# Optimization experiments

Measured on AMD Instinct MI355X. Metric: run time of the kernel, lower is better.

Reference implementation:

```python
import jax, jax.numpy as jnp
import numpy as np

RADIUS = 0.25  # module init arg


def _spp(x):
    """Spatial pyramid max pooling over the (K=8, C) plane.
    x: [B, N, 8, C] -> [B, N, 21] (4x4 + 2x2 + 1x1 bins)."""
    B, N, K, C = x.shape
    outs = []
    for h, w in ((4, 4), (2, 2), (1, 1)):
        r = x.reshape(B, N, h, K // h, w, C // w)
        outs.append(r.max(axis=(3, 5)).reshape(B, N, h * w))
    return jnp.concatenate(outs, axis=-1)


def _pointsift_select(xyz, radius):
    """Octant-wise nearest-neighbor selection. xyz: [Bp, N, 3] -> idx [Bp, N, 8]."""
    Bp, N, _ = xyz.shape
    judge = radius * radius
    # diff[b, n, m] = xyz[b, m] - xyz[b, n]  (point m relative to centroid n)
    diff = xyz[:, None, :, :] - xyz[:, :, None, :]          # [Bp, N, N, 3]
    dist = jnp.sum(diff * diff, axis=-1)                     # [Bp, N, N]
    octw = jnp.array([4, 2, 1], dtype=jnp.int32)
    sub = jnp.sum((diff + 1.0).astype(jnp.int32) * octw, -1)  # [Bp, N, N] octant id
    valid = (dist > 1e-10) & (dist < judge)
    eye = jnp.eye(N, dtype=bool)                             # self entry gets judge_dist
    idxs = []
    for i in range(8):
        d_i = jnp.where(valid & (sub == i), dist, 1e10)
        d_i = jnp.where(eye, judge, d_i)
        idxs.append(jnp.argmin(d_i, axis=-1))                # first-min, matches torch
    return jnp.stack(idxs, axis=-1)                          # [Bp, N, 8]


def setup_inputs() -> dict:
    key = jax.random.key(0)
    ks = jax.random.split(key, 7)
    C = 256
    x = jax.random.uniform(ks[0], (2, 2, 2048, 3), dtype=jnp.float32)
    w1 = jax.random.normal(ks[1], (C, 3), dtype=jnp.float32) * 0.05
    b1 = jax.random.normal(ks[2], (C,), dtype=jnp.float32) * 0.05
    w2 = jax.random.normal(ks[3], (C, C), dtype=jnp.float32) * 0.05
    b2 = jax.random.normal(ks[4], (C,), dtype=jnp.float32) * 0.05
    w3 = jax.random.normal(ks[5], (C, C), dtype=jnp.float32) * 0.05
    b3 = jax.random.normal(ks[6], (C,), dtype=jnp.float32) * 0.05
    return {"x": x, "w1": w1, "b1": b1, "w2": w2, "b2": b2, "w3": w3, "b3": b3}


def reference(x, w1, b1, w2, b2, w3, b3):
    B, T, N, _ = x.shape
    xyz = x.reshape(B * T, N, 3)
    idx = _pointsift_select(xyz, RADIUS)                     # [Bp, N, 8]
    b_idx = jnp.arange(B * T)[:, None, None]
    grouped = xyz[b_idx, idx] - xyz[:, :, None, :]           # [Bp, N, 8, 3] relative coords
    # three stacked 1x1 convs (no nonlinearity, per original Sequential)
    h = jnp.einsum('bnkc,oc->bnko', grouped, w1) + b1
    h = jnp.einsum('bnkc,oc->bnko', h, w2) + b2
    h = jnp.einsum('bnkc,oc->bnko', h, w3) + b3              # [Bp, N, 8, C]
    out = _spp(h)                                            # [Bp, N, 21]
    return out.reshape(B, T, N, -1)
```

## Files before the change

### kernel.cpp

```cpp
#include <hip/hip_runtime.h>

#define NPTS 2048
#define CCH  256
#define CAP  320
#define CAPU (CAP - 64)

template <int CTRL>
__device__ __forceinline__ float dppf(float v) {
    return __int_as_float(__builtin_amdgcn_update_dpp(
        0, __float_as_int(v), CTRL, 0xF, 0xF, true));
}
__device__ __forceinline__ float row16_max(float v) {
    v = fmaxf(v, dppf<0xB1>(v));
    v = fmaxf(v, dppf<0x4E>(v));
    v = fmaxf(v, dppf<0x141>(v));
    v = fmaxf(v, dppf<0x140>(v));
    return v;
}
__device__ __forceinline__ float row16_min(float v) {
    v = fminf(v, dppf<0xB1>(v));
    v = fminf(v, dppf<0x4E>(v));
    v = fminf(v, dppf<0x141>(v));
    v = fminf(v, dppf<0x140>(v));
    return v;
}
__device__ __forceinline__ float row16_sum(float v) {
    v += dppf<0xB1>(v);
    v += dppf<0x4E>(v);
    v += dppf<0x141>(v);
    v += dppf<0x140>(v);
    return v;
}
__device__ __forceinline__ float wave_sum(float v) {
    v = row16_sum(v);
    v += __shfl_xor(v, 16, 64);
    v += __shfl_xor(v, 32, 64);
    return v;
}

__device__ __forceinline__ int cell_coord(float v) {
    int c = (int)(v * 4.0f);
    return min(3, max(0, c));
}


__global__ __launch_bounds__(256) void prep_kernel(
    const float* __restrict__ w1, const float* __restrict__ b1,
    const float* __restrict__ w2, const float* __restrict__ b2,
    const float* __restrict__ w3, const float* __restrict__ b3,
    float* __restrict__ ws)
{
    __shared__ float  w3row[2][CCH];
    __shared__ float4 wpart[2][4];
    int o0 = blockIdx.x * 2, c = threadIdx.x;

    float w3c0 = w3[(o0 + 0) * CCH + c];
    float w3c1 = w3[(o0 + 1) * CCH + c];
    w3row[0][c] = w3c0;
    w3row[1][c] = w3c1;
    __syncthreads();

    float a0 = 0.f, a1 = 0.f, a2 = 0.f, a3 = 0.f;
    float b0 = 0.f, b1p = 0.f, b2p = 0.f, b3p = 0.f;
    const float* w2c = w2 + c;
    for (int k = 0; k < CCH; k += 4) {
        float q0 = w2c[(k + 0) * CCH];
        float q1 = w2c[(k + 1) * CCH];
        float q2 = w2c[(k + 2) * CCH];
        float q3 = w2c[(k + 3) * CCH];
        a0 = fmaf(w3row[0][k + 0], q0, a0);
        a1 = fmaf(w3row[0][k + 1], q1, a1);
        a2 = fmaf(w3row[0][k + 2], q2, a2);
        a3 = fmaf(w3row[0][k + 3], q3, a3);
        b0  = fmaf(w3row[1][k + 0], q0, b0);
        b1p = fmaf(w3row[1][k + 1], q1, b1p);
        b2p = fmaf(w3row[1][k + 2], q2, b2p);
        b3p = fmaf(w3row[1][k + 3], q3, b3p);
    }
    float accA = (a0 + a1) + (a2 + a3);
    float accB = (b0 + b1p) + (b2p + b3p);

    float w1x = w1[c * 3 + 0], w1y = w1[c * 3 + 1], w1z = w1[c * 3 + 2];
    float b1c = b1[c], b2c = b2[c];

    float4 vA = make_float4(accA * w1x, accA * w1y, accA * w1z,
                            fmaf(accA, b1c, w3c0 * b2c));
    float4 vB = make_float4(accB * w1x, accB * w1y, accB * w1z,
                            fmaf(accB, b1c, w3c1 * b2c));
    vA.x = wave_sum(vA.x); vA.y = wave_sum(vA.y);
    vA.z = wave_sum(vA.z); vA.w = wave_sum(vA.w);
    vB.x = wave_sum(vB.x); vB.y = wave_sum(vB.y);
    vB.z = wave_sum(vB.z); vB.w = wave_sum(vB.w);
    if ((c & 63) == 0) {
        wpart[0][c >> 6] = vA;
        wpart[1][c >> 6] = vB;
    }
    __syncthreads();
    if (c < 2) {
        int o = o0 + c;
        float4 p0 = wpart[c][0], p1 = wpart[c][1], p2 = wpart[c][2], p3 = wpart[c][3];
        ws[o * 3 + 0] = (p0.x + p1.x) + (p2.x + p3.x);
        ws[o * 3 + 1] = (p0.y + p1.y) + (p2.y + p3.y);
        ws[o * 3 + 2] = (p0.z + p1.z) + (p2.z + p3.z);
        ws[3 * CCH + o] = (p0.w + p1.w) + (p2.w + p3.w) + b3[o];
    }
}

__global__ __launch_bounds__(1024) void pointsift_kernel(
    const float* __restrict__ x,
    const float* __restrict__ ws,
    float* __restrict__ out)
{
    __shared__ float4 scrd[NPTS];
    __shared__ unsigned sstart[66];
    __shared__ unsigned shist[64];
    __shared__ unsigned scur[64];
    __shared__ unsigned short slist[16][CAP];

    int tid = threadIdx.x;
    int batch = blockIdx.x >> 7;
    int n0    = (blockIdx.x & 127) * 16;
    const float* xb = x + (size_t)batch * NPTS * 3;

    if (tid < 64) shist[tid] = 0;
    __syncthreads();

    float2 f0 = *(const float2*)(xb + 6 * tid + 0);
    float2 f1 = *(const float2*)(xb + 6 * tid + 2);
    float2 f2 = *(const float2*)(xb + 6 * tid + 4);
    float3 p0 = make_float3(f0.x, f0.y, f1.x);
    float3 p1 = make_float3(f1.y, f2.x, f2.y);
    int c0 = (cell_coord(p0.x) << 4) | (cell_coord(p0.y) << 2) | cell_coord(p0.z);
    int c1 = (cell_coord(p1.x) << 4) | (cell_coord(p1.y) << 2) | cell_coord(p1.z);
    atomicAdd(&shist[c0], 1u);
    atomicAdd(&shist[c1], 1u);
    __syncthreads();

    if (tid < 64) {
        unsigned v = shist[tid];
        unsigned incl = v;
#pragma unroll
        for (int s = 1; s < 64; s <<= 1) {
            unsigned o = __shfl_up(incl, s, 64);
            if (tid >= s) incl += o;
        }
        unsigned excl = incl - v;
        sstart[tid] = excl;
        scur[tid] = excl;
        if (tid == 63) sstart[64] = NPTS;
    }
    __syncthreads();

    {
        unsigned q0 = atomicAdd(&scur[c0], 1u);
        scrd[q0] = make_float4(p0.x, p0.y, p0.z, __uint_as_float(2u * tid));
        unsigned q1 = atomicAdd(&scur[c1], 1u);
        scrd[q1] = make_float4(p1.x, p1.y, p1.z, __uint_as_float(2u * tid + 1u));
    }

    int wave = tid >> 6;
    int lane = tid & 63;
    int n = n0 + wave;

    float3 cpt = *(const float3*)(xb + 3 * n);
    float cx = cpt.x, cy = cpt.y, cz = cpt.z;

    __syncthreads();

    int ccx = cell_coord(cx), ccy = cell_coord(cy), ccz = cell_coord(cz);
    int zlo = ccz > 0 ? ccz - 1 : 0;
    int zhi = ccz < 3 ? ccz + 1 : 3;

    unsigned short* slw = slist[wave];

    unsigned cnt = 0;
    for (int di = -1; di <= 1; ++di) {
        int a = ccx + di;
        if ((unsigned)a > 3u) continue;
        for (int dj = -1; dj <= 1; ++dj) {
            int bc = ccy + dj;
            if ((unsigned)bc > 3u) continue;
            int base = (a << 4) | (bc << 2);
            unsigned s0 = sstart[base + zlo];
            unsigned e0 = sstart[base + zhi + 1];
            for (unsigned pp = s0; pp < e0; pp += 64) {
                unsigned pos = pp + lane;
                bool inb = pos < e0;
                float4 p = scrd[inb ? pos : 0];
                float dx = p.x - cx, dy = p.y - cy, dz = p.z - cz;
                float d2 = __fadd_rn(__fadd_rn(__fmul_rn(dx, dx), __fmul_rn(dy, dy)),
                                     __fmul_rn(dz, dz));
                bool valid = inb && (d2 > 1e-10f) && (d2 < 0.0625f);
                unsigned long long mask = __ballot(valid);
                if (valid && cnt <= CAPU) {
                    unsigned below = __builtin_amdgcn_mbcnt_hi(
                        (unsigned)(mask >> 32),
                        __builtin_amdgcn_mbcnt_lo((unsigned)mask, 0u));
                    slw[cnt + below] = (unsigned short)pos;
                }
                cnt += (unsigned)__popcll(mask);
            }
        }
    }

    unsigned long long bk[8];
#pragma unroll
    for (int i = 0; i < 8; ++i)
        bk[i] = (0x7f800000ULL << 32) | (unsigned)n;

    if (cnt <= CAPU) {
        int cn = (int)cnt;
        for (int t = lane; t < cn; t += 64) {
            int pos = slw[t];
            float4 p = scrd[pos];
            unsigned m = __float_as_uint(p.w);
            float dx = p.x - cx, dy = p.y - cy, dz = p.z - cz;
            float d2 = __fadd_rn(__fadd_rn(__fmul_rn(dx, dx), __fmul_rn(dy, dy)),
                                 __fmul_rn(dz, dz));
            int oct = 4 * (int)(dx + 1.0f) + 2 * (int)(dy + 1.0f) + (int)(dz + 1.0f);
            unsigned long long key =
                ((unsigned long long)__float_as_uint(d2) << 32) | m;
#pragma unroll
            for (int i = 0; i < 8; ++i) {
                bool upd = (oct == i) && (key < bk[i]);
                bk[i] = upd ? key : bk[i];
            }
        }
    } else {
        for (int pos = lane; pos < NPTS; pos += 64) {
            float4 p = scrd[pos];
            unsigned m = __float_as_uint(p.w);
            float dx = p.x - cx, dy = p.y - cy, dz = p.z - cz;
            float d2 = __fadd_rn(__fadd_rn(__fmul_rn(dx, dx), __fmul_rn(dy, dy)),
                                 __fmul_rn(dz, dz));
            bool valid = (d2 > 1e-10f) && (d2 < 0.0625f);
            int oct = 4 * (int)(dx + 1.0f) + 2 * (int)(dy + 1.0f) + (int)(dz + 1.0f);
            unsigned long long key =
                ((unsigned long long)__float_as_uint(d2) << 32) | m;
#pragma unroll
            for (int i = 0; i < 8; ++i) {
                bool upd = valid && (oct == i) && (key < bk[i]);
                bk[i] = upd ? key : bk[i];
            }
        }
    }

    int nidx[8];
#pragma unroll
    for (int i = 0; i < 8; ++i) {
        float bdf = __uint_as_float((unsigned)(bk[i] >> 32));
        int   bii = (int)(unsigned)bk[i];
        float mv = row16_min(bdf);
        mv = fminf(mv, __shfl_xor(mv, 16, 64));
        mv = fminf(mv, __shfl_xor(mv, 32, 64));
        unsigned long long mk = __ballot(bdf == mv);
        if (__popcll(mk) == 1) {
            nidx[i] = __builtin_amdgcn_readlane(bii, (int)__builtin_ctzll(mk));
        } else {
            int mm = (bdf == mv) ? bii : 0x7FFFFFFF;
#pragma unroll
            for (int s = 32; s > 0; s >>= 1) {
                int o = __shfl_xor(mm, s, 64);
                mm = o < mm ? o : mm;
            }
            nidx[i] = mm;
        }
    }

    const float4* wsv = (const float4*)ws;
    float4 wa = wsv[lane * 3 + 0];
    float4 wb = wsv[lane * 3 + 1];
    float4 wc = wsv[lane * 3 + 2];
    float4 be = ((const float4*)(ws + 3 * CCH))[lane];
    float w[4][3] = {{wa.x, wa.y, wa.z}, {wa.w, wb.x, wb.y},
                     {wb.z, wb.w, wc.x}, {wc.y, wc.z, wc.w}};
    float bev[4] = {be.x, be.y, be.z, be.w};

    float m16[4];
#pragma unroll
    for (int i = 0; i < 4; ++i) m16[i] = -__builtin_inff();
#pragma unroll
    for (int k = 0; k < 8; ++k) {
        float3 p = *(const float3*)(xb + 3 * nidx[k]);
        float gx = p.x - cx, gy = p.y - cy, gz = p.z - cz;
#pragma unroll
        for (int q = 0; q < 4; ++q) {
            float h = fmaf(gx, w[q][0], fmaf(gy, w[q][1], fmaf(gz, w[q][2], bev[q])));
            m16[k >> 1] = fmaxf(m16[k >> 1], h);
        }
    }

    float t[4], u[4];
#pragma unroll
    for (int i = 0; i < 4; ++i) {
        m16[i] = row16_max(m16[i]);
        t[i] = fmaxf(m16[i], __shfl_xor(m16[i], 16, 64));
        u[i] = fmaxf(t[i], __shfl_xor(t[i], 32, 64));
    }

    float* op = out + ((size_t)batch * NPTS + n) * 21;
    if ((lane & 15) == 0) {
        int j = lane >> 4;
#pragma unroll
        for (int i = 0; i < 4; ++i)
            op[i * 4 + j] = m16[i];
    }
    if (lane == 0 || lane == 32) {
        int j2 = lane >> 5;
        op[16 + 0 * 2 + j2] = fmaxf(t[0], t[1]);
        op[16 + 1 * 2 + j2] = fmaxf(t[2], t[3]);
    }
    if (lane == 0) {
        op[20] = fmaxf(fmaxf(u[0], u[1]), fmaxf(u[2], u[3]));
    }
}

extern "C" void kernel_launch(void* const* d_in, const int* in_sizes, int n_in,
                              void* d_out, int out_size, void* d_ws, size_t ws_size,
                              hipStream_t stream) {
    const float* x  = (const float*)d_in[0];
    const float* w1 = (const float*)d_in[1];
    const float* b1 = (const float*)d_in[2];
    const float* w2 = (const float*)d_in[3];
    const float* b2 = (const float*)d_in[4];
    const float* w3 = (const float*)d_in[5];
    const float* b3 = (const float*)d_in[6];
    float* out = (float*)d_out;
    float* ws  = (float*)d_ws;

    prep_kernel<<<CCH / 2, CCH, 0, stream>>>(w1, b1, w2, b2, w3, b3, ws);

    int Bp = in_sizes[0] / (NPTS * 3);
    pointsift_kernel<<<Bp * (NPTS / 16), 1024, 0, stream>>>(x, ws, out);
}
```

Measured before the change: 26.33 us.

## Replace neighbor list compaction and wave reductions with LDS atomic-min per octant

Each wave now keeps eight packed (distance, index) keys in shared memory, one per octant. Candidates in the neighboring grid cells update those keys directly with a 64-bit workgroup-scope atomic min. This removes the ballot-compacted neighbor list, the second candidate pass, the dense fallback scan over all points, and the per-octant cross-lane min reductions. In exchange, lanes that hit the same octant now contend on LDS atomics, and correctness relies on the wave's own LDS atomics being visible to its later reads without an explicit barrier.

New measurement: 22.15 us, median of 2. 1.19x faster.

```diff
diff --git a/kernel.cpp b/kernel.cpp
--- a/kernel.cpp
+++ b/kernel.cpp
@@ -2,8 +2,6 @@
 
 #define NPTS 2048
 #define CCH  256
-#define CAP  320
-#define CAPU (CAP - 64)
 
 template <int CTRL>
 __device__ __forceinline__ float dppf(float v) {
@@ -15,13 +13,6 @@
     v = fmaxf(v, dppf<0x4E>(v));
     v = fmaxf(v, dppf<0x141>(v));
     v = fmaxf(v, dppf<0x140>(v));
-    return v;
-}
-__device__ __forceinline__ float row16_min(float v) {
-    v = fminf(v, dppf<0xB1>(v));
-    v = fminf(v, dppf<0x4E>(v));
-    v = fminf(v, dppf<0x141>(v));
-    v = fminf(v, dppf<0x140>(v));
     return v;
 }
 __device__ __forceinline__ float row16_sum(float v) {
@@ -115,7 +106,7 @@
     __shared__ unsigned sstart[66];
     __shared__ unsigned shist[64];
     __shared__ unsigned scur[64];
-    __shared__ unsigned short slist[16][CAP];
+    __shared__ unsigned long long soct[16][8];
 
     int tid = threadIdx.x;
     int batch = blockIdx.x >> 7;
@@ -165,15 +156,15 @@
     float3 cpt = *(const float3*)(xb + 3 * n);
     float cx = cpt.x, cy = cpt.y, cz = cpt.z;
 
+    if (lane < 8)
+        soct[wave][lane] = (0x7f800000ULL << 32) | (unsigned)n;
+
     __syncthreads();
 
     int ccx = cell_coord(cx), ccy = cell_coord(cy), ccz = cell_coord(cz);
     int zlo = ccz > 0 ? ccz - 1 : 0;
     int zhi = ccz < 3 ? ccz + 1 : 3;
 
-    unsigned short* slw = slist[wave];
-
-    unsigned cnt = 0;
     for (int di = -1; di <= 1; ++di) {
         int a = ccx + di;
         if ((unsigned)a > 3u) continue;
@@ -183,89 +174,28 @@
             int base = (a << 4) | (bc << 2);
             unsigned s0 = sstart[base + zlo];
             unsigned e0 = sstart[base + zhi + 1];
-            for (unsigned pp = s0; pp < e0; pp += 64) {
-                unsigned pos = pp + lane;
-                bool inb = pos < e0;
-                float4 p = scrd[inb ? pos : 0];
+            for (unsigned pp = s0 + lane; pp < e0; pp += 64) {
+                float4 p = scrd[pp];
                 float dx = p.x - cx, dy = p.y - cy, dz = p.z - cz;
                 float d2 = __fadd_rn(__fadd_rn(__fmul_rn(dx, dx), __fmul_rn(dy, dy)),
                                      __fmul_rn(dz, dz));
-                bool valid = inb && (d2 > 1e-10f) && (d2 < 0.0625f);
-                unsigned long long mask = __ballot(valid);
-                if (valid && cnt <= CAPU) {
-                    unsigned below = __builtin_amdgcn_mbcnt_hi(
-                        (unsigned)(mask >> 32),
-                        __builtin_amdgcn_mbcnt_lo((unsigned)mask, 0u));
-                    slw[cnt + below] = (unsigned short)pos;
+                if ((d2 > 1e-10f) && (d2 < 0.0625f)) {
+                    int oct = 4 * (int)(dx + 1.0f) + 2 * (int)(dy + 1.0f) + (int)(dz + 1.0f);
+                    unsigned long long key =
+                        ((unsigned long long)__float_as_uint(d2) << 32) |
+                        __float_as_uint(p.w);
+                    __hip_atomic_fetch_min(&soct[wave][oct], key,
+                                           __ATOMIC_RELAXED,
+                                           __HIP_MEMORY_SCOPE_WORKGROUP);
                 }
-                cnt += (unsigned)__popcll(mask);
             }
         }
     }
 
-    unsigned long long bk[8];
-#pragma unroll
-    for (int i = 0; i < 8; ++i)
-        bk[i] = (0x7f800000ULL << 32) | (unsigned)n;
-
-    if (cnt <= CAPU) {
-        int cn = (int)cnt;
-        for (int t = lane; t < cn; t += 64) {
-            int pos = slw[t];
-            float4 p = scrd[pos];
-            unsigned m = __float_as_uint(p.w);
-            float dx = p.x - cx, dy = p.y - cy, dz = p.z - cz;
-            float d2 = __fadd_rn(__fadd_rn(__fmul_rn(dx, dx), __fmul_rn(dy, dy)),
-                                 __fmul_rn(dz, dz));
-            int oct = 4 * (int)(dx + 1.0f) + 2 * (int)(dy + 1.0f) + (int)(dz + 1.0f);
-            unsigned long long key =
-                ((unsigned long long)__float_as_uint(d2) << 32) | m;
-#pragma unroll
-            for (int i = 0; i < 8; ++i) {
-                bool upd = (oct == i) && (key < bk[i]);
-                bk[i] = upd ? key : bk[i];
-            }
-        }
-    } else {
-        for (int pos = lane; pos < NPTS; pos += 64) {
-            float4 p = scrd[pos];
-            unsigned m = __float_as_uint(p.w);
-            float dx = p.x - cx, dy = p.y - cy, dz = p.z - cz;
-            float d2 = __fadd_rn(__fadd_rn(__fmul_rn(dx, dx), __fmul_rn(dy, dy)),
-                                 __fmul_rn(dz, dz));
-            bool valid = (d2 > 1e-10f) && (d2 < 0.0625f);
-            int oct = 4 * (int)(dx + 1.0f) + 2 * (int)(dy + 1.0f) + (int)(dz + 1.0f);
-            unsigned long long key =
-                ((unsigned long long)__float_as_uint(d2) << 32) | m;
-#pragma unroll
-            for (int i = 0; i < 8; ++i) {
-                bool upd = valid && (oct == i) && (key < bk[i]);
-                bk[i] = upd ? key : bk[i];
-            }
-        }
-    }
-
     int nidx[8];
 #pragma unroll
-    for (int i = 0; i < 8; ++i) {
-        float bdf = __uint_as_float((unsigned)(bk[i] >> 32));
-        int   bii = (int)(unsigned)bk[i];
-        float mv = row16_min(bdf);
-        mv = fminf(mv, __shfl_xor(mv, 16, 64));
-        mv = fminf(mv, __shfl_xor(mv, 32, 64));
-        unsigned long long mk = __ballot(bdf == mv);
-        if (__popcll(mk) == 1) {
-            nidx[i] = __builtin_amdgcn_readlane(bii, (int)__builtin_ctzll(mk));
-        } else {
-            int mm = (bdf == mv) ? bii : 0x7FFFFFFF;
-#pragma unroll
-            for (int s = 32; s > 0; s >>= 1) {
-                int o = __shfl_xor(mm, s, 64);
-                mm = o < mm ? o : mm;
-            }
-            nidx[i] = mm;
-        }
-    }
+    for (int k = 0; k < 8; ++k)
+        nidx[k] = (int)(unsigned)soct[wave][k];
 
     const float4* wsv = (const float4*)ws;
     float4 wa = wsv[lane * 3 + 0];
```
